# Kernel tuning notes

Hardware: AMD Instinct MI355X
Metric: run time of the kernel (lower is better)

The kernel has to match this reference:

```python
import jax, jax.numpy as jnp
import numpy as np

N_HEADS = 16


def setup_inputs() -> dict:
    key = jax.random.key(0)
    k1, k2, k3 = jax.random.split(key, 3)
    B, T, C = 4, 2048, 1024
    x = jax.random.normal(k1, (B, T, C), dtype=jnp.float32)
    # nn.Linear weights: init ~ U(-1/sqrt(fan_in), 1/sqrt(fan_in)); scaled normal is fine for a reference
    w_qkv = jax.random.normal(k2, (C, 3 * C), dtype=jnp.float32) * (1.0 / np.sqrt(C))
    w_out = jax.random.normal(k3, (C, C), dtype=jnp.float32) * (1.0 / np.sqrt(C))
    return {"x": x, "w_qkv": w_qkv, "w_out": w_out}


def reference(x, w_qkv, w_out):
    B, T, C = x.shape
    H = N_HEADS
    D = C // H  # head_dim
    qkv = x @ w_qkv  # [B, T, 3C]
    q, k, v = jnp.split(qkv, 3, axis=-1)
    # [B, H, T, D]
    q = q.reshape(B, T, H, D).transpose(0, 2, 1, 3)
    k = k.reshape(B, T, H, D).transpose(0, 2, 1, 3)
    v = v.reshape(B, T, H, D).transpose(0, 2, 1, 3)
    scale = 1.0 / np.sqrt(D)
    scores = jnp.einsum('bhqd,bhkd->bhqk', q, k) * scale  # [B, H, T, T]
    causal = jnp.tril(jnp.ones((T, T), dtype=bool))
    scores = jnp.where(causal[None, None, :, :], scores, -jnp.inf)
    weights = jax.nn.softmax(scores, axis=-1)
    out = jnp.einsum('bhqk,bhkd->bhqd', weights, v)  # [B, H, T, D]
    out = out.transpose(0, 2, 1, 3).reshape(B, T, C)
    return out @ w_out
```

## Files before the change

kernel.cpp:

```cpp
#include <hip/hip_runtime.h>
#include <hip/hip_bf16.h>
#include <math.h>
#include <type_traits>

using s16x8 = __attribute__((ext_vector_type(8))) short;
using s16x4 = __attribute__((ext_vector_type(4))) short;
using f32x4 = __attribute__((ext_vector_type(4))) float;
using f32x16 = __attribute__((ext_vector_type(16))) float;
using u32 = unsigned int;
using u32x4 = __attribute__((ext_vector_type(4))) u32;

static __device__ __forceinline__ short f2bf(float f) {
  union { float f; unsigned u; } v; v.f = f;
  unsigned r = v.u + 0x7fff + ((v.u >> 16) & 1);
  return (short)(r >> 16);
}

static __device__ __forceinline__ unsigned cvt_pk_bf16(float lo, float hi) {
  unsigned r;
  asm("v_cvt_pk_bf16_f32 %0, %1, %2" : "=v"(r) : "v"(lo), "v"(hi));
  return r;
}

static __device__ __forceinline__ float fast_exp2(float x) {
  float r; asm("v_exp_f32 %0, %1" : "=v"(r) : "v"(x)); return r;
}

#define GLOAD_LDS(gsrc, ldst)                                                      \
  __builtin_amdgcn_global_load_lds(                                                \
      (const __attribute__((address_space(1))) void*)(gsrc),                       \
      (__attribute__((address_space(3))) void*)(ldst), 16, 0, 0)

__global__ void cast_f32_bf16(const float* __restrict__ in, short* __restrict__ out, int n4) {
  int i = blockIdx.x * blockDim.x + threadIdx.x;
  int stride = gridDim.x * blockDim.x;
  for (int idx = i; idx < n4; idx += stride) {
    float4 v = reinterpret_cast<const float4*>(in)[idx];
    s16x4 o; o[0] = f2bf(v.x); o[1] = f2bf(v.y); o[2] = f2bf(v.z); o[3] = f2bf(v.w);
    reinterpret_cast<s16x4*>(out)[idx] = o;
  }
}

__global__ void transpose_cast(const float* __restrict__ in, short* __restrict__ out, int R, int C) {
  __shared__ float tile[32][33];
  int cb = blockIdx.x * 32, rb = blockIdx.y * 32;
  int tx = threadIdx.x, ty = threadIdx.y;
  #pragma unroll
  for (int i = 0; i < 32; i += 8)
    tile[ty + i][tx] = in[(size_t)(rb + ty + i) * C + cb + tx];
  __syncthreads();
  #pragma unroll
  for (int i = 0; i < 32; i += 8)
    out[(size_t)(cb + ty + i) * R + rb + tx] = f2bf(tile[tx][ty + i]);
}

template <typename OutT, bool VFUSE>
__global__ __launch_bounds__(256) void gemm_bt(const short* __restrict__ A,
                                               const short* __restrict__ BT,
                                               OutT* __restrict__ C,
                                               short* __restrict__ vtOut,
                                               int M, int N, int K, int ldc) {
  __shared__ __align__(16) short As[2][128 * 64];
  __shared__ __align__(16) short Bs[2][128 * 64];
  const int t = threadIdx.x;
  const int lane = t & 63, wid = t >> 6;
  const int wm = wid >> 1, wn = wid & 1;
  const int lr = lane & 15, lg = lane >> 4;

  const int gx = gridDim.x, gy = gridDim.y;
  const int fid = blockIdx.y * gx + blockIdx.x;
  const int k8 = fid & 7;
  const int j = fid >> 3;
  const int cpx = gx >> 3;
  const int bn = (k8 * cpx + j / gy) * 128;
  const int bm = (j % gy) * 128;

  const int srow = lane >> 3;
  const int schunk = (lane & 7) ^ srow;
  const short* ap = A + (size_t)(bm + wid * 8 + srow) * K + schunk * 8;
  const short* bp = BT + (size_t)(bn + wid * 8 + srow) * K + schunk * 8;

  f32x4 acc[4][4] = {};
  const int nk = K >> 6;

  auto stage = [&](int buf, int kt) {
    const size_t ko = (size_t)kt << 6;
    #pragma unroll
    for (int jj = 0; jj < 4; ++jj) {
      GLOAD_LDS(ap + (size_t)jj * 32 * K + ko, &As[buf][(jj * 32 + wid * 8) * 64]);
      GLOAD_LDS(bp + (size_t)jj * 32 * K + ko, &Bs[buf][(jj * 32 + wid * 8) * 64]);
    }
  };

  stage(0, 0);
  for (int kt = 0; kt < nk; ++kt) {
    __syncthreads();
    if (kt + 1 < nk) stage((kt + 1) & 1, kt + 1);
    const short* A_ = &As[kt & 1][0];
    const short* B_ = &Bs[kt & 1][0];
    #pragma unroll
    for (int ks = 0; ks < 2; ++ks) {
      s16x8 af[4], bfr[4];
      #pragma unroll
      for (int i = 0; i < 4; ++i) {
        int r = wm * 64 + i * 16 + lr;
        af[i] = *reinterpret_cast<const s16x8*>(&A_[r * 64 + (((ks * 4 + lg) ^ (r & 7)) * 8)]);
      }
      #pragma unroll
      for (int jj = 0; jj < 4; ++jj) {
        int r = wn * 64 + jj * 16 + lr;
        bfr[jj] = *reinterpret_cast<const s16x8*>(&B_[r * 64 + (((ks * 4 + lg) ^ (r & 7)) * 8)]);
      }
      #pragma unroll
      for (int i = 0; i < 4; ++i)
        #pragma unroll
        for (int jj = 0; jj < 4; ++jj)
          acc[i][jj] = __builtin_amdgcn_mfma_f32_16x16x32_bf16(af[i], bfr[jj], acc[i][jj], 0, 0, 0);
    }
  }

  const int r0 = bm + wm * 64, c0 = bn + wn * 64;
  if (!VFUSE || c0 < 2048) {
    #pragma unroll
    for (int i = 0; i < 4; ++i)
      #pragma unroll
      for (int jj = 0; jj < 4; ++jj)
        #pragma unroll
        for (int r = 0; r < 4; ++r) {
          int row = r0 + i * 16 + lg * 4 + r;
          int col = c0 + jj * 16 + lr;
          float v = acc[i][jj][r];
          if constexpr (std::is_same<OutT, short>::value)
            C[(size_t)row * ldc + col] = f2bf(v);
          else
            C[(size_t)row * ldc + col] = v;
        }
  } else {
    const int bb = bm >> 11;
    #pragma unroll
    for (int i = 0; i < 4; ++i) {
      int tok = (bm & 2047) + wm * 64 + i * 16 + lg * 4;
      #pragma unroll
      for (int jj = 0; jj < 4; ++jj) {
        int col = c0 + jj * 16 + lr;
        s16x4 p;
        #pragma unroll
        for (int r = 0; r < 4; ++r) p[r] = f2bf(acc[i][jj][r]);
        *reinterpret_cast<s16x4*>(vtOut + (size_t)(bb * 1024 + col - 2048) * 2048 + tok) = p;
      }
    }
  }
}

__global__ __launch_bounds__(256, 4) void attn_kernel(const short* __restrict__ qk,
                                                      const short* __restrict__ vt,
                                                      short* __restrict__ att) {
  const int T = 2048, C2 = 2048, Cc = 1024;
  const int fid = blockIdx.x;
  const int qb = 15 - (fid >> 6);
  const int bh = fid & 63;
  const int h = bh & 15, b = bh >> 4;
  const int t = threadIdx.x;
  const int w = t >> 6, l = t & 63;
  const int q2 = l & 31, hi = l >> 5;

  __shared__ __align__(16) short Ks[2][64 * 64];
  __shared__ __align__(16) short Vts[2][64 * 64];

  const int qrow_base = qb * 128 + w * 32;
  const int qrow = qrow_base + q2;
  const int tmax = 2 * qb + (w >> 1);
  const int nt = 2 * qb + 2;

  const float SC = 0.125f * 1.44269504088896340736f;
  s16x8 aq[4];
  #pragma unroll
  for (int ds = 0; ds < 4; ++ds) {
    s16x8 q = *reinterpret_cast<const s16x8*>(
        qk + (size_t)(b * T + qrow) * C2 + h * 64 + ds * 16 + hi * 8);
    #pragma unroll
    for (int j = 0; j < 8; ++j) {
      union { float f; unsigned u; } v; v.u = ((unsigned)(unsigned short)q[j]) << 16;
      q[j] = f2bf(v.f * SC);
    }
    aq[ds] = q;
  }

  u32 off[8];
  #pragma unroll
  for (int g = 0; g < 2; ++g)
    #pragma unroll
    for (int i = 0; i < 4; ++i)
      off[g * 4 + i] = (u32)((g * 32 + q2) * 128 + (((i * 2 + hi) ^ (q2 & 7)) * 16));

  f32x16 o[2] = {};
  float mst = -INFINITY, lst = 0.f;

  const int srow = w * 16 + (l >> 3);
  const int srcc8 = ((l & 7) ^ (l >> 3)) * 8;
  const short* kp = qk + (size_t)(b * T + srow) * C2 + Cc + h * 64 + srcc8;
  const short* vp = vt + (size_t)(bh * 64 + srow) * T + srcc8;

  auto stage = [&](int buf) {
    GLOAD_LDS(kp,           &Ks[buf][(w * 16) * 64]);
    GLOAD_LDS(kp + 8 * C2,  &Ks[buf][(w * 16 + 8) * 64]);
    GLOAD_LDS(vp,           &Vts[buf][(w * 16) * 64]);
    GLOAD_LDS(vp + 8 * T,   &Vts[buf][(w * 16 + 8) * 64]);
    kp += 64 * C2;
    vp += 64;
  };

  stage(0);
  for (int tt = 0; tt < nt; ++tt) {
    __syncthreads();
    if (tt + 1 < nt) stage((tt + 1) & 1);
    if (tt > tmax) continue;
    const int j0 = tt << 6;
    const char* K_ = reinterpret_cast<const char*>(&Ks[tt & 1][0]);
    const char* V_ = reinterpret_cast<const char*>(&Vts[tt & 1][0]);

    f32x16 st[2];
    __builtin_amdgcn_s_setprio(1);
    #pragma unroll
    for (int kt = 0; kt < 2; ++kt) {
      f32x16 s = {};
      #pragma unroll
      for (int ds = 0; ds < 4; ++ds) {
        s16x8 ak = *reinterpret_cast<const s16x8*>(K_ + off[kt * 4 + ds]);
        s = __builtin_amdgcn_mfma_f32_32x32x16_bf16(ak, aq[ds], s, 0, 0, 0);
      }
      st[kt] = s;
    }
    __builtin_amdgcn_s_setprio(0);

    if (j0 + 63 > qrow_base) {
      #pragma unroll
      for (int kt = 0; kt < 2; ++kt)
        #pragma unroll
        for (int r = 0; r < 16; ++r) {
          int key = j0 + kt * 32 + (r & 3) + 8 * (r >> 2) + 4 * hi;
          if (key > qrow) st[kt][r] = -INFINITY;
        }
    }

    float a16[16];
    #pragma unroll
    for (int r = 0; r < 16; ++r) a16[r] = fmaxf(st[0][r], st[1][r]);
    #pragma unroll
    for (int r = 0; r < 8; ++r) a16[r] = fmaxf(a16[r], a16[r + 8]);
    #pragma unroll
    for (int r = 0; r < 4; ++r) a16[r] = fmaxf(a16[r], a16[r + 4]);
    float mx = fmaxf(fmaxf(a16[0], a16[1]), fmaxf(a16[2], a16[3]));
    mx = fmaxf(mx, __shfl_xor(mx, 32));
    const bool resc = !__all(mx - mst <= 8.f);
    if (resc) {
      float mn = fmaxf(mst, mx);
      float corr = fast_exp2(mst - mn);
      mst = mn;
      lst *= corr;
      #pragma unroll
      for (int dt = 0; dt < 2; ++dt)
        #pragma unroll
        for (int r = 0; r < 16; ++r) o[dt][r] *= corr;
    }
    #pragma unroll
    for (int kt = 0; kt < 2; ++kt)
      #pragma unroll
      for (int r = 0; r < 16; ++r) st[kt][r] = fast_exp2(st[kt][r] - mst);
    float sv[16];
    #pragma unroll
    for (int r = 0; r < 16; ++r) sv[r] = st[0][r] + st[1][r];
    #pragma unroll
    for (int r = 0; r < 8; ++r) sv[r] += sv[r + 8];
    #pragma unroll
    for (int r = 0; r < 4; ++r) sv[r] += sv[r + 4];
    float ps = (sv[0] + sv[1]) + (sv[2] + sv[3]);
    ps += __shfl_xor(ps, 32);
    lst += ps;

    s16x8 pb[4];
    #pragma unroll
    for (int kt = 0; kt < 2; ++kt)
      #pragma unroll
      for (int s = 0; s < 2; ++s) {
        unsigned w01 = cvt_pk_bf16(st[kt][s * 8 + 0], st[kt][s * 8 + 1]);
        unsigned w23 = cvt_pk_bf16(st[kt][s * 8 + 2], st[kt][s * 8 + 3]);
        unsigned w45 = cvt_pk_bf16(st[kt][s * 8 + 4], st[kt][s * 8 + 5]);
        unsigned w67 = cvt_pk_bf16(st[kt][s * 8 + 6], st[kt][s * 8 + 7]);
        asm("v_permlane32_swap_b32 %0, %1" : "+v"(w01), "+v"(w45));
        asm("v_permlane32_swap_b32 %0, %1" : "+v"(w23), "+v"(w67));
        u32x4 f; f[0] = w01; f[1] = w23; f[2] = w45; f[3] = w67;
        pb[kt * 2 + s] = *reinterpret_cast<s16x8*>(&f);
      }

    __builtin_amdgcn_s_setprio(1);
    #pragma unroll
    for (int dt = 0; dt < 2; ++dt) {
      #pragma unroll
      for (int ks = 0; ks < 4; ++ks) {
        s16x8 av = *reinterpret_cast<const s16x8*>(V_ + off[dt * 4 + ks]);
        o[dt] = __builtin_amdgcn_mfma_f32_32x32x16_bf16(av, pb[ks], o[dt], 0, 0, 0);
      }
    }
    __builtin_amdgcn_s_setprio(0);
  }

  __syncthreads();
  u32* osm = reinterpret_cast<u32*>(&Ks[0][0]) + w * 1024;
  float inv = 1.f / lst;
  #pragma unroll
  for (int dt = 0; dt < 2; ++dt)
    #pragma unroll
    for (int p = 0; p < 8; ++p) {
      unsigned pk = ((unsigned)(unsigned short)f2bf(o[dt][2 * p + 1] * inv) << 16)
                  | (unsigned)(unsigned short)f2bf(o[dt][2 * p] * inv);
      int col = dt * 16 + (p >> 1) * 4 + 2 * hi + (p & 1);
      int chunk = col >> 2, inc = col & 3;
      osm[q2 * 32 + ((chunk ^ (q2 & 7)) * 4) + inc] = pk;
    }
  #pragma unroll
  for (int c = 0; c < 4; ++c) {
    int chunk = hi * 4 + c;
    u32x4 v4 = *reinterpret_cast<u32x4*>(&osm[q2 * 32 + ((chunk ^ (q2 & 7)) * 4)]);
    *reinterpret_cast<u32x4*>(
        att + (size_t)(b * T + qrow_base + q2) * Cc + h * 64 + chunk * 8) = v4;
  }
}

extern "C" void kernel_launch(void* const* d_in, const int* in_sizes, int n_in,
                              void* d_out, int out_size, void* d_ws, size_t ws_size,
                              hipStream_t stream) {
  const float* x     = (const float*)d_in[0];
  const float* w_qkv = (const float*)d_in[1];
  const float* w_out = (const float*)d_in[2];
  float* out = (float*)d_out;

  char* ws = (char*)d_ws;
  short* xb    = (short*)(ws);
  short* wqkvT = (short*)(ws + 16777216);
  short* woT   = (short*)(ws + 23068672);
  short* qk    = (short*)(ws + 25165824);
  short* vtb   = (short*)(ws + 58720256);
  short* att   = (short*)(ws + 75497472);

  cast_f32_bf16<<<2048, 256, 0, stream>>>(x, xb, (8192 * 1024) / 4);
  transpose_cast<<<dim3(3072 / 32, 1024 / 32), dim3(32, 8), 0, stream>>>(w_qkv, wqkvT, 1024, 3072);
  transpose_cast<<<dim3(1024 / 32, 1024 / 32), dim3(32, 8), 0, stream>>>(w_out, woT, 1024, 1024);

  gemm_bt<short, true><<<dim3(3072 / 128, 8192 / 128), 256, 0, stream>>>(
      xb, wqkvT, qk, vtb, 8192, 3072, 1024, 2048);
  attn_kernel<<<1024, 256, 0, stream>>>(qk, vtb, att);
  gemm_bt<float, false><<<dim3(1024 / 128, 8192 / 128), 256, 0, stream>>>(
      att, woT, out, nullptr, 8192, 1024, 1024, 1024);
}
```

Measured before the change: 174.5 us.

## Enlarge GEMM tiles to 256x256 with 8 waves and interleaved prefetch pipeline

Both projection GEMMs move from 128x128 tiles with 4 waves to 256x256 tiles with 8 waves, giving each wave a 128x64 output and more data reuse per LDS load. The next k-tile's global-to-LDS loads are split into four pieces and spread across the MFMA phases. Explicit vmcnt waits, raw barriers and setprio around the MFMA blocks replace __syncthreads. The workgroup mapping is reswizzled across 8 groups. Risks: far fewer workgroups (384 and 128), which underfills the CUs on the output GEMM, plus higher register and LDS pressure.

```diff
diff --git a/kernel.cpp b/kernel.cpp
--- a/kernel.cpp
+++ b/kernel.cpp
@@ -55,74 +55,94 @@
 }
 
 template <typename OutT, bool VFUSE>
-__global__ __launch_bounds__(256) void gemm_bt(const short* __restrict__ A,
-                                               const short* __restrict__ BT,
-                                               OutT* __restrict__ C,
-                                               short* __restrict__ vtOut,
-                                               int M, int N, int K, int ldc) {
-  __shared__ __align__(16) short As[2][128 * 64];
-  __shared__ __align__(16) short Bs[2][128 * 64];
+__global__ __launch_bounds__(512, 2) void gemm256(const short* __restrict__ A,
+                                                  const short* __restrict__ BT,
+                                                  OutT* __restrict__ C,
+                                                  short* __restrict__ vtOut,
+                                                  int M, int N, int K, int ldc) {
+  __shared__ __align__(16) short As[2][256 * 64];
+  __shared__ __align__(16) short Bs[2][256 * 64];
   const int t = threadIdx.x;
-  const int lane = t & 63, wid = t >> 6;
-  const int wm = wid >> 1, wn = wid & 1;
+  const int lane = t & 63, w = t >> 6;
+  const int wm = w >> 2, wn = w & 3;
   const int lr = lane & 15, lg = lane >> 4;
 
-  const int gx = gridDim.x, gy = gridDim.y;
-  const int fid = blockIdx.y * gx + blockIdx.x;
-  const int k8 = fid & 7;
-  const int j = fid >> 3;
-  const int cpx = gx >> 3;
-  const int bn = (k8 * cpx + j / gy) * 128;
-  const int bm = (j % gy) * 128;
+  const int gx = gridDim.x;
+  const int nwg = gx * gridDim.y;
+  int fid = blockIdx.y * gx + blockIdx.x;
+  fid = (fid & 7) * (nwg >> 3) + (fid >> 3);
+  const int bn = (fid % gx) * 256;
+  const int bm = (fid / gx) * 256;
 
   const int srow = lane >> 3;
   const int schunk = (lane & 7) ^ srow;
-  const short* ap = A + (size_t)(bm + wid * 8 + srow) * K + schunk * 8;
-  const short* bp = BT + (size_t)(bn + wid * 8 + srow) * K + schunk * 8;
-
-  f32x4 acc[4][4] = {};
+  const short* ap = A + (size_t)(bm + w * 8 + srow) * K + schunk * 8;
+  const short* bp = BT + (size_t)(bn + w * 8 + srow) * K + schunk * 8;
+
+  f32x4 acc[8][4] = {};
   const int nk = K >> 6;
 
-  auto stage = [&](int buf, int kt) {
+  auto site = [&](int buf, int kt, int j) {
     const size_t ko = (size_t)kt << 6;
-    #pragma unroll
-    for (int jj = 0; jj < 4; ++jj) {
-      GLOAD_LDS(ap + (size_t)jj * 32 * K + ko, &As[buf][(jj * 32 + wid * 8) * 64]);
-      GLOAD_LDS(bp + (size_t)jj * 32 * K + ko, &Bs[buf][(jj * 32 + wid * 8) * 64]);
-    }
+    GLOAD_LDS(ap + (size_t)(j * 64) * K + ko, &As[buf][(j * 64 + w * 8) * 64]);
+    GLOAD_LDS(bp + (size_t)(j * 64) * K + ko, &Bs[buf][(j * 64 + w * 8) * 64]);
   };
 
-  stage(0, 0);
+  #pragma unroll
+  for (int j = 0; j < 4; ++j) site(0, 0, j);
+
   for (int kt = 0; kt < nk; ++kt) {
-    __syncthreads();
-    if (kt + 1 < nk) stage((kt + 1) & 1, kt + 1);
-    const short* A_ = &As[kt & 1][0];
-    const short* B_ = &Bs[kt & 1][0];
-    #pragma unroll
-    for (int ks = 0; ks < 2; ++ks) {
-      s16x8 af[4], bfr[4];
-      #pragma unroll
-      for (int i = 0; i < 4; ++i) {
-        int r = wm * 64 + i * 16 + lr;
-        af[i] = *reinterpret_cast<const s16x8*>(&A_[r * 64 + (((ks * 4 + lg) ^ (r & 7)) * 8)]);
-      }
-      #pragma unroll
-      for (int jj = 0; jj < 4; ++jj) {
+    const int cur = kt & 1, nxt = cur ^ 1;
+    const bool pf = (kt + 1 < nk);
+    if (pf) {
+      site(nxt, kt + 1, 0);
+      asm volatile("s_waitcnt vmcnt(2)" ::: "memory");
+    } else {
+      asm volatile("s_waitcnt vmcnt(0)" ::: "memory");
+    }
+    __builtin_amdgcn_s_barrier();
+    __builtin_amdgcn_sched_barrier(0);
+    const short* A_ = &As[cur][0];
+    const short* B_ = &Bs[cur][0];
+    s16x8 bfr[4][2];
+    #pragma unroll
+    for (int jj = 0; jj < 4; ++jj)
+      #pragma unroll
+      for (int ks = 0; ks < 2; ++ks) {
         int r = wn * 64 + jj * 16 + lr;
-        bfr[jj] = *reinterpret_cast<const s16x8*>(&B_[r * 64 + (((ks * 4 + lg) ^ (r & 7)) * 8)]);
-      }
-      #pragma unroll
-      for (int i = 0; i < 4; ++i)
+        bfr[jj][ks] = *reinterpret_cast<const s16x8*>(
+            &B_[r * 64 + (((ks * 4 + lg) ^ (r & 7)) * 8)]);
+      }
+    #pragma unroll
+    for (int p = 0; p < 4; ++p) {
+      if (p && pf) site(nxt, kt + 1, p);
+      s16x8 af[2][2];
+      #pragma unroll
+      for (int ii = 0; ii < 2; ++ii)
+        #pragma unroll
+        for (int ks = 0; ks < 2; ++ks) {
+          int r = wm * 128 + (p * 2 + ii) * 16 + lr;
+          af[ii][ks] = *reinterpret_cast<const s16x8*>(
+              &A_[r * 64 + (((ks * 4 + lg) ^ (r & 7)) * 8)]);
+        }
+      __builtin_amdgcn_s_setprio(1);
+      #pragma unroll
+      for (int ii = 0; ii < 2; ++ii)
         #pragma unroll
         for (int jj = 0; jj < 4; ++jj)
-          acc[i][jj] = __builtin_amdgcn_mfma_f32_16x16x32_bf16(af[i], bfr[jj], acc[i][jj], 0, 0, 0);
-    }
-  }
-
-  const int r0 = bm + wm * 64, c0 = bn + wn * 64;
+          #pragma unroll
+          for (int ks = 0; ks < 2; ++ks)
+            acc[p * 2 + ii][jj] = __builtin_amdgcn_mfma_f32_16x16x32_bf16(
+                af[ii][ks], bfr[jj][ks], acc[p * 2 + ii][jj], 0, 0, 0);
+      __builtin_amdgcn_s_setprio(0);
+      __builtin_amdgcn_s_barrier();
+    }
+  }
+
+  const int r0 = bm + wm * 128, c0 = bn + wn * 64;
   if (!VFUSE || c0 < 2048) {
     #pragma unroll
-    for (int i = 0; i < 4; ++i)
+    for (int i = 0; i < 8; ++i)
       #pragma unroll
       for (int jj = 0; jj < 4; ++jj)
         #pragma unroll
@@ -138,8 +158,8 @@
   } else {
     const int bb = bm >> 11;
     #pragma unroll
-    for (int i = 0; i < 4; ++i) {
-      int tok = (bm & 2047) + wm * 64 + i * 16 + lg * 4;
+    for (int i = 0; i < 8; ++i) {
+      int tok = (bm & 2047) + wm * 128 + i * 16 + lg * 4;
       #pragma unroll
       for (int jj = 0; jj < 4; ++jj) {
         int col = c0 + jj * 16 + lr;
@@ -347,9 +367,9 @@
   transpose_cast<<<dim3(3072 / 32, 1024 / 32), dim3(32, 8), 0, stream>>>(w_qkv, wqkvT, 1024, 3072);
   transpose_cast<<<dim3(1024 / 32, 1024 / 32), dim3(32, 8), 0, stream>>>(w_out, woT, 1024, 1024);
 
-  gemm_bt<short, true><<<dim3(3072 / 128, 8192 / 128), 256, 0, stream>>>(
+  gemm256<short, true><<<dim3(3072 / 256, 8192 / 256), 512, 0, stream>>>(
       xb, wqkvT, qk, vtb, 8192, 3072, 1024, 2048);
   attn_kernel<<<1024, 256, 0, stream>>>(qk, vtb, att);
-  gemm_bt<float, false><<<dim3(1024 / 128, 8192 / 128), 256, 0, stream>>>(
+  gemm256<float, false><<<dim3(1024 / 256, 8192 / 256), 512, 0, stream>>>(
       att, woT, out, nullptr, 8192, 1024, 1024, 1024);
 }
```

Measured after the change: 224.6 us. 28.7% more time.
